# Kernel tuning notes

Measured on AMD Instinct MI355X. Metric: run time of the kernel, lower is better.

Reference implementation:

```python
import jax, jax.numpy as jnp
import numpy as np

N, D, P = 4096, 1024, 2048
TAU, ALPHA = 0.2, 0.8
GAMMA_EX, GAMMA_IN = 2.0, 1.6
EPS = 1e-8


def _cos_sim(e):
    # F.cosine_similarity(e[:,None], e[None,:], dim=2) == normalized rows matmul
    n = jnp.linalg.norm(e, axis=1, keepdims=True)
    en = e / jnp.maximum(n, EPS)
    return en @ en.T  # [N, N]


def setup_inputs() -> dict:
    key = jax.random.key(0)
    embeddings = jax.random.normal(key, (N, D), dtype=jnp.float32)
    # positive pairs: (0,1),(2,3),... (arange fill)
    pp = np.arange(2 * P).reshape(P, 2)
    pos_partner = np.arange(N)
    pos_partner[pp[:, 0]] = pp[:, 1]
    pos_partner[pp[:, 1]] = pp[:, 0]
    # negative pairs = all ordered (i,j), i!=j, minus ordered positive tuples,
    # enumerated row-major (deterministic stand-in for torch's set order).
    pos_m = np.zeros((N, N), dtype=bool)
    pos_m[pp[:, 0], pp[:, 1]] = True
    neg_m = ~np.eye(N, dtype=bool) & ~pos_m
    ii, jj = np.nonzero(neg_m)  # row-major order
    neg_partner = np.arange(N)
    neg_partner[ii] = jj
    neg_partner[jj] = ii  # processed[j] = ... overwrites after
    return {
        "embeddings": embeddings,
        "positive_pairs": jnp.asarray(pp, jnp.int32),
        "pos_partner": jnp.asarray(pos_partner, jnp.int32),
        "neg_partner": jnp.asarray(neg_partner, jnp.int32),
    }


def reference(embeddings, positive_pairs, pos_partner, neg_partner):
    pi, pj = positive_pairs[:, 0], positive_pairs[:, 1]
    # Beta(gamma,gamma) scalar mixing coefficients (dim_mixing=False)
    lam_pos = jax.random.beta(jax.random.key(1), GAMMA_EX, GAMMA_EX) + 1.0  # 'ex'
    lam_neg = jax.random.beta(jax.random.key(2), GAMMA_IN, GAMMA_IN)        # 'in'

    orig = _cos_sim(embeddings)
    hp = _cos_sim(lam_pos * embeddings + (1.0 - lam_pos) * embeddings[pos_partner])
    hn = _cos_sim(lam_neg * embeddings + (1.0 - lam_neg) * embeddings[neg_partner])

    eye = jnp.eye(N, dtype=bool)
    pos_m = jnp.zeros((N, N), dtype=bool).at[pi, pj].set(True)  # ordered positives
    neg_m = ~eye & ~pos_m                                        # ordered negatives
    # pos replacement first, then neg replacement overwrites (faithful ordering)
    sim = jnp.where(pos_m | pos_m.T, hp, orig)
    sim = jnp.where(neg_m | neg_m.T, hn, sim)

    # ----- compute_loss (stage='train': quantile hard-negative mining) -----
    mask = eye | pos_m | pos_m.T
    exp_sim = jnp.exp(sim / TAU)
    exp_masked = jnp.where(mask, 0.0, exp_sim)
    pos_ij = exp_sim[pi, pj]
    pos_ji = exp_sim[pj, pi]
    exp_i = exp_masked[pi]  # [P, N]
    exp_j = exp_masked[pj]
    thr_i = jnp.quantile(exp_i, ALPHA, axis=1, keepdims=True)
    thr_j = jnp.quantile(exp_j, ALPHA, axis=1, keepdims=True)
    sum_i = jnp.where(exp_i >= thr_i, exp_i, 0.0).sum(axis=1)
    sum_j = jnp.where(exp_j >= thr_j, exp_j, 0.0).sum(axis=1)
    loss_ij = -jnp.log(pos_ij / (pos_ij + sum_i))
    loss_ji = -jnp.log(pos_ji / (pos_ji + sum_j))
    return (loss_ij + loss_ji).sum() / (2 * P)
```

## Files before the change

kernel.cpp:

```cpp
#include <hip/hip_runtime.h>
#include <hip/hip_bf16.h>

#define NN 4096
#define DD 1024
constexpr float LAM = 0.45f;
constexpr float INV_TAU = 5.0f;
constexpr int KSEL = 820;
constexpr unsigned KEY_BASE = 0x3B80u;
constexpr int NBINS = 2048;

typedef __attribute__((ext_vector_type(8))) short bf16x8;
typedef __attribute__((ext_vector_type(4))) float f32x4;

__device__ inline void async_copy16(const ushort* g, ushort* l) {
    __builtin_amdgcn_global_load_lds(
        (const __attribute__((address_space(1))) void*)g,
        (__attribute__((address_space(3))) void*)l, 16, 0, 0);
}

__global__ __launch_bounds__(256) void mixnorm_kernel(const float* __restrict__ E,
                                                      const int* __restrict__ negp,
                                                      ushort* __restrict__ U) {
    int r = blockIdx.x, t = threadIdx.x;
    int p = negp[r];
    const float a = LAM, b = 1.0f - LAM;
    float4 x = ((const float4*)(E + (size_t)r * DD))[t];
    float4 y = ((const float4*)(E + (size_t)p * DD))[t];
    float4 m;
    m.x = a * x.x + b * y.x;
    m.y = a * x.y + b * y.y;
    m.z = a * x.z + b * y.z;
    m.w = a * x.w + b * y.w;
    float ss = m.x * m.x + m.y * m.y + m.z * m.z + m.w * m.w;
    #pragma unroll
    for (int off = 32; off > 0; off >>= 1) ss += __shfl_down(ss, off, 64);
    __shared__ float part[4];
    if ((t & 63) == 0) part[t >> 6] = ss;
    __syncthreads();
    float tot = part[0] + part[1] + part[2] + part[3];
    float inv = 1.0f / fmaxf(sqrtf(tot), 1e-8f);
    ushort4 o;
    o.x = __bfloat16_as_ushort(__float2bfloat16(m.x * inv));
    o.y = __bfloat16_as_ushort(__float2bfloat16(m.y * inv));
    o.z = __bfloat16_as_ushort(__float2bfloat16(m.z * inv));
    o.w = __bfloat16_as_ushort(__float2bfloat16(m.w * inv));
    ((ushort4*)(U + (size_t)r * DD))[t] = o;
}

__global__ __launch_bounds__(256) void gemm_exp_kernel(const ushort* __restrict__ U,
                                                       ushort* __restrict__ Z) {
    __shared__ ushort sm_all[8192 + 9216];
    ushort* As = sm_all;
    ushort* Bs = sm_all + 4096;
    const int t = threadIdx.x;
    const int w = t >> 6, l = t & 63;

    const int m = blockIdx.x;
    float fdec = sqrtf(8.0f * (float)m + 1.0f);
    int by = (int)((fdec - 1.0f) * 0.5f);
    while ((by + 1) * (by + 2) / 2 <= m) by++;
    while (by * (by + 1) / 2 > m) by--;
    const int bx = m - by * (by + 1) / 2;

    const ushort* gA = U + (size_t)(by * 128 + (t >> 2)) * DD + (t & 3) * 8;
    const ushort* gB = U + (size_t)(bx * 128 + (t >> 2)) * DD + (t & 3) * 8;
    ushort* lA0 = As + w * 512;
    ushort* lA1 = As + 2048 + w * 512;
    ushort* lB0 = Bs + w * 512;
    ushort* lB1 = Bs + 2048 + w * 512;

    f32x4 acc[4][4];
    #pragma unroll
    for (int i = 0; i < 4; i++)
        #pragma unroll
        for (int j = 0; j < 4; j++) acc[i][j] = (f32x4){0.f, 0.f, 0.f, 0.f};

    const int mrow = ((w >> 1) << 6) + (l & 15);
    const int nrow = ((w & 1) << 6) + (l & 15);
    const int kq = (l >> 4) * 8;

    for (int k0 = 0; k0 < DD; k0 += 32) {
        async_copy16(gA, lA0);
        async_copy16(gA + 64 * DD, lA1);
        async_copy16(gB, lB0);
        async_copy16(gB + 64 * DD, lB1);
        gA += 32; gB += 32;
        __syncthreads();
        bf16x8 af[4], bfr[4];
        #pragma unroll
        for (int i = 0; i < 4; i++)
            af[i] = *(const bf16x8*)(As + (mrow + i * 16) * 32 + kq);
        #pragma unroll
        for (int j = 0; j < 4; j++)
            bfr[j] = *(const bf16x8*)(Bs + (nrow + j * 16) * 32 + kq);
        __syncthreads();
        #pragma unroll
        for (int i = 0; i < 4; i++)
            #pragma unroll
            for (int j = 0; j < 4; j++)
                acc[i][j] = __builtin_amdgcn_mfma_f32_16x16x32_bf16(af[i], bfr[j], acc[i][j], 0, 0, 0);
    }

    ushort* smv = sm_all;
    ushort* smT = sm_all + 8192;
    const int wr = w >> 1, wc = w & 1;
    const bool mirror = (bx != by);
    #pragma unroll
    for (int h = 0; h < 2; h++) {
        __syncthreads();
        if (wr == h) {
            #pragma unroll
            for (int i = 0; i < 4; i++)
                #pragma unroll
                for (int j = 0; j < 4; j++)
                    #pragma unroll
                    for (int rg = 0; rg < 4; rg++) {
                        float v = __expf(acc[i][j][rg] * INV_TAU);
                        ushort hv = __bfloat16_as_ushort(__float2bfloat16(v));
                        int lrow = i * 16 + ((l >> 4) << 2) + rg;
                        int lcol = (wc << 6) + j * 16 + (l & 15);
                        smv[lrow * 128 + lcol] = hv;
                        smT[lcol * 72 + lrow] = hv;
                    }
        }
        __syncthreads();
        {
            int lrow = t >> 2;
            int ucol = (t & 3) * 32;
            const uint4* src = (const uint4*)(smv + lrow * 128 + ucol);
            uint4* dst = (uint4*)(Z + (size_t)(by * 128 + h * 64 + lrow) * NN + bx * 128 + ucol);
            #pragma unroll
            for (int q = 0; q < 4; q++) dst[q] = src[q];
        }
        if (mirror) {
            int c = t >> 1, seg = t & 1;
            const uint4* srcT = (const uint4*)(smT + c * 72 + seg * 32);
            uint4* dstT = (uint4*)(Z + (size_t)(bx * 128 + c) * NN + by * 128 + h * 64 + seg * 32);
            #pragma unroll
            for (int q = 0; q < 4; q++) dstT[q] = srcT[q];
        }
    }
}

__global__ __launch_bounds__(256) void rowloss_kernel(const ushort* __restrict__ Z,
                                                      const int* __restrict__ posp,
                                                      float* __restrict__ loss) {
    __shared__ unsigned histall[4][NBINS / 2];
    const int t = threadIdx.x, w = t >> 6, l = t & 63;
    const int r = blockIdx.x * 4 + w;
    unsigned* hist = histall[w];
    const int p = posp[r];
    const uint4* zr = (const uint4*)(Z + (size_t)r * NN);

    #pragma unroll
    for (int q = 0; q < 4; q++) ((uint4*)hist)[l * 4 + q] = (uint4){0u, 0u, 0u, 0u};

    const float posv = __uint_as_float(((unsigned)Z[(size_t)r * NN + p]) << 16);

    #pragma unroll 4
    for (int c = 0; c < 16; c++) {
        uint4 v = zr[c * 64 + l];
        unsigned wd[4] = {v.x, v.y, v.z, v.w};
        const int cb = (c * 64 + l) * 8;
        #pragma unroll
        for (int q = 0; q < 4; q++) {
            unsigned lo = wd[q] & 0xFFFFu;
            unsigned hi = wd[q] >> 16;
            int c0 = cb + 2 * q, c1 = c0 + 1;
            lo = (c0 == p || c0 == r) ? 0u : lo;
            hi = (c1 == p || c1 == r) ? 0u : hi;
            int b0 = max(0, min(NBINS - 1, (int)lo - (int)KEY_BASE));
            int b1 = max(0, min(NBINS - 1, (int)hi - (int)KEY_BASE));
            atomicAdd(&hist[b0 >> 1], 1u << ((b0 & 1) * 16));
            atomicAdd(&hist[b1 >> 1], 1u << ((b1 & 1) * 16));
        }
    }

    unsigned ow[16];
    {
        const uint4* hv = (const uint4*)(hist + l * 16);
        #pragma unroll
        for (int q = 0; q < 4; q++) {
            uint4 x = hv[q];
            ow[4 * q] = x.x; ow[4 * q + 1] = x.y; ow[4 * q + 2] = x.z; ow[4 * q + 3] = x.w;
        }
    }
    unsigned lsum = 0;
    #pragma unroll
    for (int i = 0; i < 16; i++) lsum += (ow[i] & 0xFFFFu) + (ow[i] >> 16);
    unsigned S = lsum;
    #pragma unroll
    for (int d = 1; d < 64; d <<= 1) {
        unsigned o = __shfl_down(S, d, 64);
        if (l + d < 64) S += o;
    }
    const bool cross = (S >= (unsigned)KSEL) && (S - lsum) < (unsigned)KSEL;
    int bstar = 0;
    if (cross) {
        int rem = KSEL - (int)(S - lsum);
        int a2 = 0;
        #pragma unroll
        for (int i = 31; i >= 0; i--) {
            unsigned c = (ow[i >> 1] >> ((i & 1) * 16)) & 0xFFFFu;
            a2 += (int)c;
            if (a2 >= rem) { bstar = l * 32 + i; break; }
        }
    }
    unsigned long long bm = __ballot(cross);
    int src = __ffsll((long long)bm) - 1;
    bstar = __shfl(bstar, src, 64);

    float s = 0.f;
    #pragma unroll
    for (int i = 0; i < 32; i++) {
        int g = l * 32 + i;
        unsigned c = (ow[i >> 1] >> ((i & 1) * 16)) & 0xFFFFu;
        if (g >= bstar && c) {
            float val = __uint_as_float((KEY_BASE + (unsigned)g) << 16);
            s = fmaf((float)c, val, s);
        }
    }
    #pragma unroll
    for (int off = 32; off > 0; off >>= 1) s += __shfl_down(s, off, 64);
    if (l == 0) loss[r] = log1pf(s / posv);
}

__global__ __launch_bounds__(256) void finalize_kernel(const float* __restrict__ loss,
                                                       unsigned* __restrict__ out) {
    __shared__ float part[4];
    const int t = threadIdx.x, w = t >> 6, l = t & 63;
    float s = 0.f;
    #pragma unroll
    for (int q = 0; q < 4; q++) {
        float4 v = ((const float4*)loss)[t * 4 + q];
        s += (v.x + v.y) + (v.z + v.w);
    }
    #pragma unroll
    for (int off = 32; off > 0; off >>= 1) s += __shfl_down(s, off, 64);
    if (l == 0) part[w] = s;
    __syncthreads();
    if (t == 0) {
        float v = (part[0] + part[1] + part[2] + part[3]) * (1.0f / 4096.0f);
        unsigned short bits = __bfloat16_as_ushort(__float2bfloat16(v));
        *out = ((unsigned)bits << 16) | (unsigned)bits;
    }
}

extern "C" void kernel_launch(void* const* d_in, const int* in_sizes, int n_in,
                              void* d_out, int out_size, void* d_ws, size_t ws_size,
                              hipStream_t stream) {
    const float* E = (const float*)d_in[0];
    const int* posp = (const int*)d_in[2];
    const int* negp = (const int*)d_in[3];

    float* loss = (float*)d_ws;
    ushort* U = (ushort*)((char*)d_ws + 16384);
    ushort* Z = (ushort*)((char*)d_ws + 16384 + (size_t)NN * DD * 2);

    mixnorm_kernel<<<NN, 256, 0, stream>>>(E, negp, U);
    gemm_exp_kernel<<<528, 256, 0, stream>>>(U, Z);
    rowloss_kernel<<<NN / 4, 256, 0, stream>>>(Z, posp, loss);
    finalize_kernel<<<1, 256, 0, stream>>>(loss, (unsigned*)d_out);
}
```

Before: 132.9 us.

## Split GEMM tile across 8 waves with smaller per-wave accumulator

The symmetric GEMM+exp kernel now launches 512 threads per block instead of 256, so each of 8 waves computes a 32x64 sub-tile (2x4 MFMA tiles) rather than a 64x64 one. Each thread issues one async copy per matrix per k-step, and the epilogue writes out in four 32-row passes with a smaller transposed staging buffer. The aim is more waves to hide latency and fewer accumulator registers per thread. In exchange each wave gets less fragment reuse, and the extra epilogue passes add more barriers.

```diff
diff --git a/kernel.cpp b/kernel.cpp
--- a/kernel.cpp
+++ b/kernel.cpp
@@ -47,9 +47,9 @@
     ((ushort4*)(U + (size_t)r * DD))[t] = o;
 }
 
-__global__ __launch_bounds__(256) void gemm_exp_kernel(const ushort* __restrict__ U,
+__global__ __launch_bounds__(512) void gemm_exp_kernel(const ushort* __restrict__ U,
                                                        ushort* __restrict__ Z) {
-    __shared__ ushort sm_all[8192 + 9216];
+    __shared__ ushort sm_all[10240];
     ushort* As = sm_all;
     ushort* Bs = sm_all + 4096;
     const int t = threadIdx.x;
@@ -64,53 +64,49 @@
 
     const ushort* gA = U + (size_t)(by * 128 + (t >> 2)) * DD + (t & 3) * 8;
     const ushort* gB = U + (size_t)(bx * 128 + (t >> 2)) * DD + (t & 3) * 8;
-    ushort* lA0 = As + w * 512;
-    ushort* lA1 = As + 2048 + w * 512;
-    ushort* lB0 = Bs + w * 512;
-    ushort* lB1 = Bs + 2048 + w * 512;
-
-    f32x4 acc[4][4];
-    #pragma unroll
-    for (int i = 0; i < 4; i++)
+    ushort* lA = As + w * 512;
+    ushort* lB = Bs + w * 512;
+
+    f32x4 acc[2][4];
+    #pragma unroll
+    for (int i = 0; i < 2; i++)
         #pragma unroll
         for (int j = 0; j < 4; j++) acc[i][j] = (f32x4){0.f, 0.f, 0.f, 0.f};
 
-    const int mrow = ((w >> 1) << 6) + (l & 15);
-    const int nrow = ((w & 1) << 6) + (l & 15);
+    const int wr = w >> 1, wc = w & 1;
+    const int mrow = wr * 32 + (l & 15);
+    const int nrow = wc * 64 + (l & 15);
     const int kq = (l >> 4) * 8;
 
     for (int k0 = 0; k0 < DD; k0 += 32) {
-        async_copy16(gA, lA0);
-        async_copy16(gA + 64 * DD, lA1);
-        async_copy16(gB, lB0);
-        async_copy16(gB + 64 * DD, lB1);
+        async_copy16(gA, lA);
+        async_copy16(gB, lB);
         gA += 32; gB += 32;
         __syncthreads();
-        bf16x8 af[4], bfr[4];
-        #pragma unroll
-        for (int i = 0; i < 4; i++)
+        bf16x8 af[2], bfr[4];
+        #pragma unroll
+        for (int i = 0; i < 2; i++)
             af[i] = *(const bf16x8*)(As + (mrow + i * 16) * 32 + kq);
         #pragma unroll
         for (int j = 0; j < 4; j++)
             bfr[j] = *(const bf16x8*)(Bs + (nrow + j * 16) * 32 + kq);
         __syncthreads();
         #pragma unroll
-        for (int i = 0; i < 4; i++)
+        for (int i = 0; i < 2; i++)
             #pragma unroll
             for (int j = 0; j < 4; j++)
                 acc[i][j] = __builtin_amdgcn_mfma_f32_16x16x32_bf16(af[i], bfr[j], acc[i][j], 0, 0, 0);
     }
 
     ushort* smv = sm_all;
-    ushort* smT = sm_all + 8192;
-    const int wr = w >> 1, wc = w & 1;
+    ushort* smT = sm_all + 4096;
     const bool mirror = (bx != by);
     #pragma unroll
-    for (int h = 0; h < 2; h++) {
+    for (int h = 0; h < 4; h++) {
         __syncthreads();
         if (wr == h) {
             #pragma unroll
-            for (int i = 0; i < 4; i++)
+            for (int i = 0; i < 2; i++)
                 #pragma unroll
                 for (int j = 0; j < 4; j++)
                     #pragma unroll
@@ -120,24 +116,19 @@
                         int lrow = i * 16 + ((l >> 4) << 2) + rg;
                         int lcol = (wc << 6) + j * 16 + (l & 15);
                         smv[lrow * 128 + lcol] = hv;
-                        smT[lcol * 72 + lrow] = hv;
+                        smT[lcol * 48 + lrow] = hv;
                     }
         }
         __syncthreads();
         {
-            int lrow = t >> 2;
-            int ucol = (t & 3) * 32;
-            const uint4* src = (const uint4*)(smv + lrow * 128 + ucol);
-            uint4* dst = (uint4*)(Z + (size_t)(by * 128 + h * 64 + lrow) * NN + bx * 128 + ucol);
-            #pragma unroll
-            for (int q = 0; q < 4; q++) dst[q] = src[q];
+            const uint4* src = (const uint4*)(smv + (t >> 4) * 128 + (t & 15) * 8);
+            uint4* dst = (uint4*)(Z + (size_t)(by * 128 + h * 32 + (t >> 4)) * NN + bx * 128 + (t & 15) * 8);
+            *dst = *src;
         }
         if (mirror) {
-            int c = t >> 1, seg = t & 1;
-            const uint4* srcT = (const uint4*)(smT + c * 72 + seg * 32);
-            uint4* dstT = (uint4*)(Z + (size_t)(bx * 128 + c) * NN + by * 128 + h * 64 + seg * 32);
-            #pragma unroll
-            for (int q = 0; q < 4; q++) dstT[q] = srcT[q];
+            const uint4* srcT = (const uint4*)(smT + (t >> 2) * 48 + (t & 3) * 8);
+            uint4* dstT = (uint4*)(Z + (size_t)(bx * 128 + (t >> 2)) * NN + by * 128 + h * 32 + (t & 3) * 8);
+            *dstT = *srcT;
         }
     }
 }
@@ -258,7 +249,7 @@
     ushort* Z = (ushort*)((char*)d_ws + 16384 + (size_t)NN * DD * 2);
 
     mixnorm_kernel<<<NN, 256, 0, stream>>>(E, negp, U);
-    gemm_exp_kernel<<<528, 256, 0, stream>>>(U, Z);
+    gemm_exp_kernel<<<528, 512, 0, stream>>>(U, Z);
     rowloss_kernel<<<NN / 4, 256, 0, stream>>>(Z, posp, loss);
     finalize_kernel<<<1, 256, 0, stream>>>(loss, (unsigned*)d_out);
 }
```

Measured after the change: 129.4 us. 2.7% less time.
